# Kernel optimization log

Measured on AMD Instinct MI355X. Metric: run time of the kernel, lower is better.

The kernel has to match this reference:

```python
import jax, jax.numpy as jnp
import numpy as np

# ---- dims / case constants ----
B, NZ, H = 2048, 128, 1000.0          # columns, vertical levels, depth [m]
NT, N_OUT, DT = 400, 40, 50.0          # steps, output stride, timestep [s]
FCOR = 1.0e-4                          # Coriolis frequency [1/s]
TFLX_SFC, SFLX_SFC = -5.0e-5, 1.0e-6   # surface tracer fluxes [K m/s, psu m/s]
TFLX_BTM, SFLX_BTM = 0.0, 0.0
RFLX_SFC = 3.7e-5                      # max solar radiative flux [K m/s]
USTR_SFC, VSTR_SFC = 1.0e-4, 0.0       # kinematic wind stress [m^2/s^2]
USTR_BTM, VSTR_BTM = 0.0, 0.0
CP = 3985.0                            # seawater heat capacity [J/kg/K]


def setup_inputs() -> dict:
    key = jax.random.key(0)
    ks = jax.random.split(key, 7)
    u = 0.1 * jax.random.normal(ks[0], (B, NZ), jnp.float32)
    v = 0.1 * jax.random.normal(ks[1], (B, NZ), jnp.float32)
    t = 20.0 + jax.random.normal(ks[2], (B, NZ), jnp.float32)
    s = 35.0 + 0.1 * jax.random.normal(ks[3], (B, NZ), jnp.float32)
    akv = 1e-5 + 1e-2 * jax.random.uniform(ks[4], (B, NZ + 1), jnp.float32)
    akt = 1e-5 + 1e-2 * jax.random.uniform(ks[5], (B, NZ + 1), jnp.float32)
    eps = 1e-9 + 1e-7 * jax.random.uniform(ks[6], (B, NZ + 1), jnp.float32)
    hz = jnp.full((NZ,), H / NZ, jnp.float32)
    return {"u": u, "v": v, "t": t, "s": s, "akv": akv, "akt": akt, "eps": eps, "hz": hz}


def lmd_swfrac(hz):
    # Paulson & Simpson two-band shortwave absorption at w-points (Jerlov I)
    zw = jnp.concatenate([jnp.array([-jnp.sum(hz)], hz.dtype), jnp.cumsum(hz) - jnp.sum(hz)])
    r1, mu1, mu2 = 0.58, 0.35, 23.0
    return r1 * jnp.exp(zw / mu1) + (1.0 - r1) * jnp.exp(zw / mu2)  # (nz+1,)


def tridiag_solve(a, b, c, d):
    # Thomas algorithm along last axis; a,b,c,d: (B, nz), vectorized over batch
    aT, bT, cT, dT = a.T, b.T, c.T, d.T  # (nz, B)
    zero = jnp.zeros_like(bT[0])

    def fwd(carry, abcd):
        cp_p, dp_p = carry
        ak, bk, ck, dk = abcd
        den = bk - ak * cp_p
        cp = ck / den
        dp = (dk - ak * dp_p) / den
        return (cp, dp), (cp, dp)

    _, (cps, dps) = jax.lax.scan(fwd, (zero, zero), (aT, bT, cT, dT))

    def bwd(x_next, cd):
        cp, dp = cd
        x = dp - cp * x_next
        return x, x

    _, xs = jax.lax.scan(bwd, zero, (cps, dps), reverse=True)
    return xs.T


def _diff_matrix(K, hz):
    # implicit vertical diffusion (I - dt*D); K at w-points (B, nz+1)
    dzw = 0.5 * (hz[:-1] + hz[1:])                       # (nz-1,) center spacing
    a = jnp.pad(-DT * K[:, 1:NZ] / (hz[1:] * dzw), ((0, 0), (1, 0)))
    c = jnp.pad(-DT * K[:, 1:NZ] / (hz[:-1] * dzw), ((0, 0), (0, 1)))
    b = 1.0 - a - c
    return a, b, c


def reference(u, v, t, s, akv, akt, eps, hz):
    swr_frac = lmd_swfrac(hz)
    at, bt, ct = _diff_matrix(akt, hz)   # tracer diffusion (closure diffusivities held fixed)
    am, bm, cm = _diff_matrix(akv, hz)   # momentum diffusion

    # tracer forcing: penetrative solar + surface/bottom fluxes + dissipation heating
    fc = RFLX_SFC * swr_frac                              # (nz+1,)
    div_t = (fc[1:] - fc[:-1]) / hz                       # (nz,)
    div_t = div_t.at[-1].add(TFLX_SFC / hz[-1]).at[0].add(-TFLX_BTM / hz[0])
    eps_c = 0.5 * (eps[:, :-1] + eps[:, 1:])              # (B, nz)
    frc_t = DT * (div_t + eps_c / CP)                     # (B, nz)
    frc_s = DT * (jnp.zeros((NZ,), hz.dtype).at[-1].add(SFLX_SFC / hz[-1]).at[0].add(-SFLX_BTM / hz[0]))

    g = DT * FCOR
    inv = 1.0 / (1.0 + g * g)

    def step(state):
        u_, v_, t_, s_ = state
        t_new = tridiag_solve(at, bt, ct, t_ + frc_t)
        s_new = tridiag_solve(at, bt, ct, s_ + frc_s)
        # semi-implicit Coriolis rotation
        u1 = (u_ + g * v_) * inv
        v1 = (v_ - g * u_) * inv
        ru = u1.at[:, -1].add(DT * USTR_SFC / hz[-1]).at[:, 0].add(-DT * USTR_BTM / hz[0])
        rv = v1.at[:, -1].add(DT * VSTR_SFC / hz[-1]).at[:, 0].add(-DT * VSTR_BTM / hz[0])
        u_new = tridiag_solve(am, bm, cm, ru)
        v_new = tridiag_solve(am, bm, cm, rv)
        return (u_new, v_new, t_new, s_new)

    def chunk(state, _):
        snap = jnp.stack(state)  # record state BEFORE the block (i_t % n_out == 0)
        def inner(st, __):
            return step(st), None
        state2, _ = jax.lax.scan(inner, state, None, length=N_OUT)
        return state2, snap

    _, snaps = jax.lax.scan(chunk, (u, v, t, s), None, length=NT // N_OUT)
    return jnp.transpose(snaps, (1, 0, 2, 3))  # (4 fields u,v,t,s ; n_snap ; B ; nz)
```

## Files before the change

kernel.cpp:

```cpp
#include <hip/hip_runtime.h>
#include <math.h>


namespace {
constexpr int NZv   = 128;
constexpr int Bv    = 2048;
constexpr int NOUTv = 40;
constexpr int NSNAP = 10;
constexpr float DTf      = 50.0f;
constexpr float FCORf    = 1.0e-4f;
constexpr float TFLX_SFC = -5.0e-5f;
constexpr float SFLX_SFC = 1.0e-6f;
constexpr float RFLX_SFC = 3.7e-5f;
constexpr float USTR_SFC = 1.0e-4f;
constexpr float CPf      = 3985.0f;

template <int CTRL>
__device__ __forceinline__ float dpp_zero(float x) {
  return __int_as_float(__builtin_amdgcn_update_dpp(
      0, __float_as_int(x), CTRL, 0xF, 0xF, true));
}
constexpr int ROW_SHR1 = 0x111, ROW_SHL1 = 0x101;
}

__global__ void __launch_bounds__(256)
__attribute__((amdgpu_waves_per_eu(2, 2)))
scm_kernel(
    const float* __restrict__ u_in, const float* __restrict__ v_in,
    const float* __restrict__ t_in, const float* __restrict__ s_in,
    const float* __restrict__ akv,  const float* __restrict__ akt,
    const float* __restrict__ eps,  const float* __restrict__ hz,
    float* __restrict__ out) {
  __shared__ float zw[NZv + 1];
  __shared__ float sh_abc[4][2][3][NZv];
  __shared__ float sh_cpp[4][2][2][NZv];

  const int tid     = threadIdx.x;
  const int lane    = tid & 63;
  const int wid     = tid >> 6;
  const bool isM    = (wid & 1) != 0;
  const int half    = lane >> 5;
  const int seg     = (lane >> 4) & 1;
  const int segLane = lane & 15;
  const int cpair   = blockIdx.x * 2 + (wid >> 1);
  const int col     = cpair * 2 + seg;
  const int k0      = segLane * 8;

  if (tid == 0) {
    float tot = 0.f;
    for (int k = 0; k < NZv; ++k) tot += hz[k];
    float run = 0.f;
    zw[0] = -tot;
    for (int k = 0; k < NZv; ++k) { run += hz[k]; zw[k + 1] = run - tot; }
  }
  __syncthreads();

  const float* Kp = isM ? akv : akt;
  float a_[8], c_[8], b_[8], hzv[8];
#pragma unroll
  for (int j = 0; j < 8; ++j) {
    const int k = k0 + j;
    const float hzk = hz[k];
    hzv[j] = hzk;
    const float Kk  = Kp[col * (NZv + 1) + k];
    const float Kk1 = Kp[col * (NZv + 1) + k + 1];
    float aj = 0.f, cj = 0.f;
    if (k > 0)       { const float dzm = 0.5f * (hz[k - 1] + hzk); aj = -DTf * Kk  / (hzk * dzm); }
    if (k < NZv - 1) { const float dzp = 0.5f * (hzk + hz[k + 1]); cj = -DTf * Kk1 / (hzk * dzp); }
    a_[j] = aj; c_[j] = cj; b_[j] = 1.f - aj - cj;
  }
  if (half == 0) {
#pragma unroll
    for (int j = 0; j < 8; ++j) {
      sh_abc[wid][seg][0][k0 + j] = a_[j];
      sh_abc[wid][seg][1][k0 + j] = b_[j];
      sh_abc[wid][seg][2][k0 + j] = c_[j];
    }
  }
  __syncthreads();
  if (half == 0 && segLane == 0) {
    float cpp = 0.f;
    for (int k = 0; k < NZv; ++k) {
      const float aa = sh_abc[wid][seg][0][k];
      const float bb = sh_abc[wid][seg][1][k];
      const float cc = sh_abc[wid][seg][2][k];
      const float den = bb - aa * cpp;
      const float pp  = 1.f / den;
      const float cpk = cc * pp;
      sh_cpp[wid][seg][0][k] = cpk;
      sh_cpp[wid][seg][1][k] = pp;
      cpp = cpk;
    }
  }
  __syncthreads();

  float p_[8], Ab_[8], A_[8];
#pragma unroll
  for (int j = 0; j < 8; ++j) {
    Ab_[j] = -sh_cpp[wid][seg][0][k0 + j];
    p_[j]  =  sh_cpp[wid][seg][1][k0 + j];
    A_[j]  = -a_[j] * p_[j];
  }
  float Ap[7];
  Ap[0] = A_[0];
#pragma unroll
  for (int j = 1; j < 7; ++j) Ap[j] = A_[j] * Ap[j - 1];

  float Absuf[8];
  Absuf[7] = Ab_[7];
#pragma unroll
  for (int j = 6; j >= 0; --j) Absuf[j] = Ab_[j] * Absuf[j + 1];

  float frc[8];
  const float hz_top = hz[NZv - 1];
  if (!isM) {
    if (half == 0) {
#pragma unroll
      for (int j = 0; j < 8; ++j) {
        const int k = k0 + j;
        const float zk = zw[k], zk1 = zw[k + 1];
        const float fck  = RFLX_SFC * (0.58f * expf(zk  * (1.f / 0.35f)) + 0.42f * expf(zk  * (1.f / 23.f)));
        const float fck1 = RFLX_SFC * (0.58f * expf(zk1 * (1.f / 0.35f)) + 0.42f * expf(zk1 * (1.f / 23.f)));
        float div = (fck1 - fck) / hzv[j];
        if (k == NZv - 1) div += TFLX_SFC / hz_top;
        const float ec = 0.5f * (eps[col * (NZv + 1) + k] + eps[col * (NZv + 1) + k + 1]);
        frc[j] = DTf * (div + ec * (1.f / CPf));
      }
    } else {
#pragma unroll
      for (int j = 0; j < 8; ++j)
        frc[j] = (k0 + j == NZv - 1) ? DTf * SFLX_SFC / hz_top : 0.f;
    }
  } else {
#pragma unroll
    for (int j = 0; j < 8; ++j) frc[j] = 0.f;
    if (half == 0 && segLane == 15) frc[7] = DTf * USTR_SFC / hz_top;
  }

  const float g    = DTf * FCORf;
  const float cinv = 1.f / (1.f + g * g);
  const float sgng = (half == 0) ? g : -g;
  float pci[8], pcg[8], pfm[8];
#pragma unroll
  for (int j = 0; j < 8; ++j) {
    if (isM) { pci[j] = p_[j] * cinv; pcg[j] = pci[j] * sgng; }
    else     { pci[j] = p_[j];        pcg[j] = 0.f; }
    pfm[j] = p_[j] * frc[j];
  }

  const float* fp = isM ? (half ? v_in : u_in) : (half ? s_in : t_in);
  float st[8];
  {
    const float4 lo = *(const float4*)(fp + (size_t)col * NZv + k0);
    const float4 hi = *(const float4*)(fp + (size_t)col * NZv + k0 + 4);
    st[0] = lo.x; st[1] = lo.y; st[2] = lo.z; st[3] = lo.w;
    st[4] = hi.x; st[5] = hi.y; st[6] = hi.z; st[7] = hi.w;
  }
  const int fidx = isM ? half : 2 + half;
  float* outb = out + ((size_t)fidx * NSNAP * Bv + col) * NZv + k0;

  auto sweep = [&](const float* in_) {
    float P[8];
    P[0] = in_[0];
#pragma unroll
    for (int j = 1; j < 8; ++j) P[j] = fmaf(A_[j], P[j - 1], in_[j]);
    const float X = dpp_zero<ROW_SHR1>(P[7]);
    float dp[8];
    dp[7] = P[7];
#pragma unroll
    for (int j = 0; j < 7; ++j) dp[j] = fmaf(Ap[j], X, P[j]);
    float Sp[8];
    Sp[7] = dp[7];
#pragma unroll
    for (int j = 6; j >= 0; --j) Sp[j] = fmaf(Ab_[j], Sp[j + 1], dp[j]);
    const float Xb = dpp_zero<ROW_SHL1>(Sp[0]);
    st[0] = Sp[0];
#pragma unroll
    for (int j = 1; j < 8; ++j) st[j] = fmaf(Absuf[j], Xb, Sp[j]);
  };

  if (!isM) {
#pragma unroll 1
    for (int ch = 0; ch < NSNAP; ++ch) {
      float* ob = outb + (size_t)ch * Bv * NZv;
      *(float4*)(ob)     = make_float4(st[0], st[1], st[2], st[3]);
      *(float4*)(ob + 4) = make_float4(st[4], st[5], st[6], st[7]);
#pragma unroll 1
      for (int it = 0; it < NOUTv; ++it) {
        float in_[8];
#pragma unroll
        for (int j = 0; j < 8; ++j) in_[j] = fmaf(pci[j], st[j], pfm[j]);
        sweep(in_);
      }
    }
  } else {
#pragma unroll 1
    for (int ch = 0; ch < NSNAP; ++ch) {
      float* ob = outb + (size_t)ch * Bv * NZv;
      *(float4*)(ob)     = make_float4(st[0], st[1], st[2], st[3]);
      *(float4*)(ob + 4) = make_float4(st[4], st[5], st[6], st[7]);
#pragma unroll 1
      for (int it = 0; it < NOUTv; ++it) {
        float in_[8];
#pragma unroll
        for (int j = 0; j < 8; ++j) {
          const float oth = __shfl_xor(st[j], 32);
          in_[j] = fmaf(pci[j], st[j], fmaf(pcg[j], oth, pfm[j]));
        }
        sweep(in_);
      }
    }
  }
}

extern "C" void kernel_launch(void* const* d_in, const int* in_sizes, int n_in,
                              void* d_out, int out_size, void* d_ws, size_t ws_size,
                              hipStream_t stream) {
  const float* u   = (const float*)d_in[0];
  const float* v   = (const float*)d_in[1];
  const float* t   = (const float*)d_in[2];
  const float* s   = (const float*)d_in[3];
  const float* akv = (const float*)d_in[4];
  const float* akt = (const float*)d_in[5];
  const float* eps = (const float*)d_in[6];
  const float* hz  = (const float*)d_in[7];
  (void)in_sizes; (void)n_in; (void)d_ws; (void)ws_size; (void)out_size;
  scm_kernel<<<dim3(Bv / 4), dim3(256), 0, stream>>>(
      u, v, t, s, akv, akt, eps, hz, (float*)d_out);
}
```

Baseline: 170.1 us.

## Process paired fields per thread to remove cross-half shuffles and duplicate precompute

Each lane now holds both fields of a pair (u and v, or t and s) for one column, so the Coriolis coupling needs no cross-lane shuffle and the two independent tridiagonal sweeps interleave for more instruction-level parallelism. Each wave now covers four columns instead of two, so the grid is halved and waves_per_eu drops to 1. This doubles register use per lane and lowers occupancy, relying on ILP to hide latency. The per-column Thomas precompute is also no longer duplicated across halves.

```diff
diff --git a/kernel.cpp b/kernel.cpp
--- a/kernel.cpp
+++ b/kernel.cpp
@@ -24,7 +24,7 @@
 }
 
 __global__ void __launch_bounds__(256)
-__attribute__((amdgpu_waves_per_eu(2, 2)))
+__attribute__((amdgpu_waves_per_eu(1, 1)))
 scm_kernel(
     const float* __restrict__ u_in, const float* __restrict__ v_in,
     const float* __restrict__ t_in, const float* __restrict__ s_in,
@@ -32,18 +32,16 @@
     const float* __restrict__ eps,  const float* __restrict__ hz,
     float* __restrict__ out) {
   __shared__ float zw[NZv + 1];
-  __shared__ float sh_abc[4][2][3][NZv];
-  __shared__ float sh_cpp[4][2][2][NZv];
+  __shared__ float sh_abc[4][4][3][NZv];
+  __shared__ float sh_cpp[4][4][2][NZv];
 
   const int tid     = threadIdx.x;
   const int lane    = tid & 63;
   const int wid     = tid >> 6;
   const bool isM    = (wid & 1) != 0;
-  const int half    = lane >> 5;
-  const int seg     = (lane >> 4) & 1;
+  const int row     = lane >> 4;
   const int segLane = lane & 15;
-  const int cpair   = blockIdx.x * 2 + (wid >> 1);
-  const int col     = cpair * 2 + seg;
+  const int col     = blockIdx.x * 8 + (wid >> 1) * 4 + row;
   const int k0      = segLane * 8;
 
   if (tid == 0) {
@@ -69,26 +67,24 @@
     if (k < NZv - 1) { const float dzp = 0.5f * (hzk + hz[k + 1]); cj = -DTf * Kk1 / (hzk * dzp); }
     a_[j] = aj; c_[j] = cj; b_[j] = 1.f - aj - cj;
   }
-  if (half == 0) {
-#pragma unroll
-    for (int j = 0; j < 8; ++j) {
-      sh_abc[wid][seg][0][k0 + j] = a_[j];
-      sh_abc[wid][seg][1][k0 + j] = b_[j];
-      sh_abc[wid][seg][2][k0 + j] = c_[j];
-    }
+#pragma unroll
+  for (int j = 0; j < 8; ++j) {
+    sh_abc[wid][row][0][k0 + j] = a_[j];
+    sh_abc[wid][row][1][k0 + j] = b_[j];
+    sh_abc[wid][row][2][k0 + j] = c_[j];
   }
   __syncthreads();
-  if (half == 0 && segLane == 0) {
+  if (segLane == 0) {
     float cpp = 0.f;
     for (int k = 0; k < NZv; ++k) {
-      const float aa = sh_abc[wid][seg][0][k];
-      const float bb = sh_abc[wid][seg][1][k];
-      const float cc = sh_abc[wid][seg][2][k];
+      const float aa = sh_abc[wid][row][0][k];
+      const float bb = sh_abc[wid][row][1][k];
+      const float cc = sh_abc[wid][row][2][k];
       const float den = bb - aa * cpp;
       const float pp  = 1.f / den;
       const float cpk = cc * pp;
-      sh_cpp[wid][seg][0][k] = cpk;
-      sh_cpp[wid][seg][1][k] = pp;
+      sh_cpp[wid][row][0][k] = cpk;
+      sh_cpp[wid][row][1][k] = pp;
       cpp = cpk;
     }
   }
@@ -97,117 +93,141 @@
   float p_[8], Ab_[8], A_[8];
 #pragma unroll
   for (int j = 0; j < 8; ++j) {
-    Ab_[j] = -sh_cpp[wid][seg][0][k0 + j];
-    p_[j]  =  sh_cpp[wid][seg][1][k0 + j];
+    Ab_[j] = -sh_cpp[wid][row][0][k0 + j];
+    p_[j]  =  sh_cpp[wid][row][1][k0 + j];
     A_[j]  = -a_[j] * p_[j];
   }
   float Ap[7];
   Ap[0] = A_[0];
 #pragma unroll
   for (int j = 1; j < 7; ++j) Ap[j] = A_[j] * Ap[j - 1];
-
   float Absuf[8];
   Absuf[7] = Ab_[7];
 #pragma unroll
   for (int j = 6; j >= 0; --j) Absuf[j] = Ab_[j] * Absuf[j + 1];
 
-  float frc[8];
   const float hz_top = hz[NZv - 1];
-  if (!isM) {
-    if (half == 0) {
-#pragma unroll
-      for (int j = 0; j < 8; ++j) {
-        const int k = k0 + j;
-        const float zk = zw[k], zk1 = zw[k + 1];
-        const float fck  = RFLX_SFC * (0.58f * expf(zk  * (1.f / 0.35f)) + 0.42f * expf(zk  * (1.f / 23.f)));
-        const float fck1 = RFLX_SFC * (0.58f * expf(zk1 * (1.f / 0.35f)) + 0.42f * expf(zk1 * (1.f / 23.f)));
-        float div = (fck1 - fck) / hzv[j];
-        if (k == NZv - 1) div += TFLX_SFC / hz_top;
-        const float ec = 0.5f * (eps[col * (NZv + 1) + k] + eps[col * (NZv + 1) + k + 1]);
-        frc[j] = DTf * (div + ec * (1.f / CPf));
-      }
-    } else {
-#pragma unroll
-      for (int j = 0; j < 8; ++j)
-        frc[j] = (k0 + j == NZv - 1) ? DTf * SFLX_SFC / hz_top : 0.f;
-    }
-  } else {
-#pragma unroll
-    for (int j = 0; j < 8; ++j) frc[j] = 0.f;
-    if (half == 0 && segLane == 15) frc[7] = DTf * USTR_SFC / hz_top;
-  }
-
   const float g    = DTf * FCORf;
   const float cinv = 1.f / (1.f + g * g);
-  const float sgng = (half == 0) ? g : -g;
-  float pci[8], pcg[8], pfm[8];
-#pragma unroll
-  for (int j = 0; j < 8; ++j) {
-    if (isM) { pci[j] = p_[j] * cinv; pcg[j] = pci[j] * sgng; }
-    else     { pci[j] = p_[j];        pcg[j] = 0.f; }
-    pfm[j] = p_[j] * frc[j];
-  }
-
-  const float* fp = isM ? (half ? v_in : u_in) : (half ? s_in : t_in);
-  float st[8];
+  float pfA[8];
+  float pfB7;
+  float pci[8], pcg[8];
+  if (!isM) {
+#pragma unroll
+    for (int j = 0; j < 8; ++j) {
+      const int k = k0 + j;
+      const float zk = zw[k], zk1 = zw[k + 1];
+      const float fck  = RFLX_SFC * (0.58f * expf(zk  * (1.f / 0.35f)) + 0.42f * expf(zk  * (1.f / 23.f)));
+      const float fck1 = RFLX_SFC * (0.58f * expf(zk1 * (1.f / 0.35f)) + 0.42f * expf(zk1 * (1.f / 23.f)));
+      float div = (fck1 - fck) / hzv[j];
+      if (k == NZv - 1) div += TFLX_SFC / hz_top;
+      const float ec = 0.5f * (eps[col * (NZv + 1) + k] + eps[col * (NZv + 1) + k + 1]);
+      pfA[j] = p_[j] * (DTf * (div + ec * (1.f / CPf)));
+      pci[j] = p_[j];
+      pcg[j] = 0.f;
+    }
+    pfB7 = (segLane == 15) ? p_[7] * (DTf * SFLX_SFC / hz_top) : 0.f;
+  } else {
+#pragma unroll
+    for (int j = 0; j < 8; ++j) {
+      pfA[j] = 0.f;
+      pci[j] = p_[j] * cinv;
+      pcg[j] = pci[j] * g;
+    }
+    if (segLane == 15) pfA[7] = p_[7] * (DTf * USTR_SFC / hz_top);
+    pfB7 = 0.f;
+  }
+
+  const float* fpA = isM ? u_in : t_in;
+  const float* fpB = isM ? v_in : s_in;
+  float stA[8], stB[8];
   {
-    const float4 lo = *(const float4*)(fp + (size_t)col * NZv + k0);
-    const float4 hi = *(const float4*)(fp + (size_t)col * NZv + k0 + 4);
-    st[0] = lo.x; st[1] = lo.y; st[2] = lo.z; st[3] = lo.w;
-    st[4] = hi.x; st[5] = hi.y; st[6] = hi.z; st[7] = hi.w;
-  }
-  const int fidx = isM ? half : 2 + half;
-  float* outb = out + ((size_t)fidx * NSNAP * Bv + col) * NZv + k0;
-
-  auto sweep = [&](const float* in_) {
-    float P[8];
-    P[0] = in_[0];
-#pragma unroll
-    for (int j = 1; j < 8; ++j) P[j] = fmaf(A_[j], P[j - 1], in_[j]);
-    const float X = dpp_zero<ROW_SHR1>(P[7]);
-    float dp[8];
-    dp[7] = P[7];
-#pragma unroll
-    for (int j = 0; j < 7; ++j) dp[j] = fmaf(Ap[j], X, P[j]);
-    float Sp[8];
-    Sp[7] = dp[7];
-#pragma unroll
-    for (int j = 6; j >= 0; --j) Sp[j] = fmaf(Ab_[j], Sp[j + 1], dp[j]);
-    const float Xb = dpp_zero<ROW_SHL1>(Sp[0]);
-    st[0] = Sp[0];
-#pragma unroll
-    for (int j = 1; j < 8; ++j) st[j] = fmaf(Absuf[j], Xb, Sp[j]);
+    const float4 alo = *(const float4*)(fpA + (size_t)col * NZv + k0);
+    const float4 ahi = *(const float4*)(fpA + (size_t)col * NZv + k0 + 4);
+    stA[0] = alo.x; stA[1] = alo.y; stA[2] = alo.z; stA[3] = alo.w;
+    stA[4] = ahi.x; stA[5] = ahi.y; stA[6] = ahi.z; stA[7] = ahi.w;
+    const float4 blo = *(const float4*)(fpB + (size_t)col * NZv + k0);
+    const float4 bhi = *(const float4*)(fpB + (size_t)col * NZv + k0 + 4);
+    stB[0] = blo.x; stB[1] = blo.y; stB[2] = blo.z; stB[3] = blo.w;
+    stB[4] = bhi.x; stB[5] = bhi.y; stB[6] = bhi.z; stB[7] = bhi.w;
+  }
+  const int fidxA = isM ? 0 : 2;
+  const int fidxB = isM ? 1 : 3;
+  float* outA = out + ((size_t)fidxA * NSNAP * Bv + col) * NZv + k0;
+  float* outB = out + ((size_t)fidxB * NSNAP * Bv + col) * NZv + k0;
+
+  auto sweep2 = [&](const float* inA, const float* inB) {
+    float PA[8], PB[8];
+    PA[0] = inA[0]; PB[0] = inB[0];
+#pragma unroll
+    for (int j = 1; j < 8; ++j) {
+      PA[j] = fmaf(A_[j], PA[j - 1], inA[j]);
+      PB[j] = fmaf(A_[j], PB[j - 1], inB[j]);
+    }
+    const float XfA = dpp_zero<ROW_SHR1>(PA[7]);
+    const float XfB = dpp_zero<ROW_SHR1>(PB[7]);
+    float dA[8], dB[8];
+    dA[7] = PA[7]; dB[7] = PB[7];
+#pragma unroll
+    for (int j = 0; j < 7; ++j) {
+      dA[j] = fmaf(Ap[j], XfA, PA[j]);
+      dB[j] = fmaf(Ap[j], XfB, PB[j]);
+    }
+    float SA[8], SB[8];
+    SA[7] = dA[7]; SB[7] = dB[7];
+#pragma unroll
+    for (int j = 6; j >= 0; --j) {
+      SA[j] = fmaf(Ab_[j], SA[j + 1], dA[j]);
+      SB[j] = fmaf(Ab_[j], SB[j + 1], dB[j]);
+    }
+    const float XbA = dpp_zero<ROW_SHL1>(SA[0]);
+    const float XbB = dpp_zero<ROW_SHL1>(SB[0]);
+    stA[0] = SA[0]; stB[0] = SB[0];
+#pragma unroll
+    for (int j = 1; j < 8; ++j) {
+      stA[j] = fmaf(Absuf[j], XbA, SA[j]);
+      stB[j] = fmaf(Absuf[j], XbB, SB[j]);
+    }
   };
 
   if (!isM) {
 #pragma unroll 1
     for (int ch = 0; ch < NSNAP; ++ch) {
-      float* ob = outb + (size_t)ch * Bv * NZv;
-      *(float4*)(ob)     = make_float4(st[0], st[1], st[2], st[3]);
-      *(float4*)(ob + 4) = make_float4(st[4], st[5], st[6], st[7]);
+      float* oa = outA + (size_t)ch * Bv * NZv;
+      float* ob = outB + (size_t)ch * Bv * NZv;
+      *(float4*)(oa)     = make_float4(stA[0], stA[1], stA[2], stA[3]);
+      *(float4*)(oa + 4) = make_float4(stA[4], stA[5], stA[6], stA[7]);
+      *(float4*)(ob)     = make_float4(stB[0], stB[1], stB[2], stB[3]);
+      *(float4*)(ob + 4) = make_float4(stB[4], stB[5], stB[6], stB[7]);
 #pragma unroll 1
       for (int it = 0; it < NOUTv; ++it) {
-        float in_[8];
-#pragma unroll
-        for (int j = 0; j < 8; ++j) in_[j] = fmaf(pci[j], st[j], pfm[j]);
-        sweep(in_);
+        float inA[8], inB[8];
+#pragma unroll
+        for (int j = 0; j < 8; ++j) {
+          inA[j] = fmaf(pci[j], stA[j], pfA[j]);
+          inB[j] = fmaf(pci[j], stB[j], (j == 7) ? pfB7 : 0.f);
+        }
+        sweep2(inA, inB);
       }
     }
   } else {
 #pragma unroll 1
     for (int ch = 0; ch < NSNAP; ++ch) {
-      float* ob = outb + (size_t)ch * Bv * NZv;
-      *(float4*)(ob)     = make_float4(st[0], st[1], st[2], st[3]);
-      *(float4*)(ob + 4) = make_float4(st[4], st[5], st[6], st[7]);
+      float* oa = outA + (size_t)ch * Bv * NZv;
+      float* ob = outB + (size_t)ch * Bv * NZv;
+      *(float4*)(oa)     = make_float4(stA[0], stA[1], stA[2], stA[3]);
+      *(float4*)(oa + 4) = make_float4(stA[4], stA[5], stA[6], stA[7]);
+      *(float4*)(ob)     = make_float4(stB[0], stB[1], stB[2], stB[3]);
+      *(float4*)(ob + 4) = make_float4(stB[4], stB[5], stB[6], stB[7]);
 #pragma unroll 1
       for (int it = 0; it < NOUTv; ++it) {
-        float in_[8];
+        float inA[8], inB[8];
 #pragma unroll
         for (int j = 0; j < 8; ++j) {
-          const float oth = __shfl_xor(st[j], 32);
-          in_[j] = fmaf(pci[j], st[j], fmaf(pcg[j], oth, pfm[j]));
+          inA[j] = fmaf(pci[j], stA[j], fmaf(pcg[j], stB[j], pfA[j]));
+          inB[j] = fmaf(pci[j], stB[j], -(pcg[j] * stA[j]));
         }
-        sweep(in_);
+        sweep2(inA, inB);
       }
     }
   }
@@ -225,6 +245,6 @@
   const float* eps = (const float*)d_in[6];
   const float* hz  = (const float*)d_in[7];
   (void)in_sizes; (void)n_in; (void)d_ws; (void)ws_size; (void)out_size;
-  scm_kernel<<<dim3(Bv / 4), dim3(256), 0, stream>>>(
+  scm_kernel<<<dim3(Bv / 8), dim3(256), 0, stream>>>(
       u, v, t, s, akv, akt, eps, hz, (float*)d_out);
 }
```

Measured after the change: 156.8 us. 7.8% less time.
